# Kernel tuning notes

Measured on AMD Instinct MI355X. Metric: run time of the kernel, lower is better.

## Reference

```python
import jax, jax.numpy as jnp
import numpy as np

N = 250_000        # nodes
E = 8_000_000      # directed edges
F_IN = 16          # dataset.num_features
H = 8              # latent_dim
G = 512            # number of graphs in the batch


def setup_inputs() -> dict:
    key = jax.random.key(0)
    k = jax.random.split(key, 9)
    x = jax.random.normal(k[0], (N, F_IN), dtype=jnp.float32)
    edge_index = jax.random.randint(k[1], (2, E), 0, N, dtype=jnp.int64)
    batch = jnp.sort(jax.random.randint(k[2], (N,), 0, G, dtype=jnp.int64))
    W1 = jax.random.normal(k[3], (F_IN, H), dtype=jnp.float32) * 0.25
    b1 = jax.random.normal(k[4], (H,), dtype=jnp.float32) * 0.1
    W2 = jax.random.normal(k[5], (H, H), dtype=jnp.float32) * 0.35
    b2 = jax.random.normal(k[6], (H,), dtype=jnp.float32) * 0.1
    Wl = jax.random.normal(k[7], (H, 1), dtype=jnp.float32) * 0.35
    bl = jax.random.normal(k[8], (1,), dtype=jnp.float32) * 0.1
    return {"x": x, "edge_index": edge_index, "batch": batch,
            "W1": W1, "b1": b1, "W2": W2, "b2": b2, "Wl": Wl, "bl": bl}


def _gcn_conv(x, src, dst, deg_inv_sqrt, W, b, num_nodes):
    # PyG GCNConv (default): h = x @ W ; msg = norm * h[src] ; scatter-add to dst ; + bias
    h = x @ W                                    # [N, H]
    norm = deg_inv_sqrt[src] * deg_inv_sqrt[dst]  # [E+N]
    msgs = h[src] * norm[:, None]                 # [E+N, H]
    out = jax.ops.segment_sum(msgs, dst, num_segments=num_nodes)
    return out + b


def reference(x, edge_index, batch, W1, b1, W2, b2, Wl, bl):
    num_nodes = x.shape[0]
    loops = jnp.arange(num_nodes, dtype=edge_index.dtype)
    src = jnp.concatenate([edge_index[0], loops])  # self-loops appended
    dst = jnp.concatenate([edge_index[1], loops])
    # symmetric normalization: deg over destination (incl. self-loops)
    deg = jax.ops.segment_sum(jnp.ones_like(dst, dtype=x.dtype), dst,
                              num_segments=num_nodes)
    dis = jnp.where(deg > 0, jax.lax.rsqrt(jnp.maximum(deg, 1.0)), 0.0)
    h = jax.nn.relu(_gcn_conv(x, src, dst, dis, W1, b1, num_nodes))
    h = jax.nn.relu(_gcn_conv(h, src, dst, dis, W2, b2, num_nodes))
    pooled = jax.ops.segment_sum(h, batch, num_segments=G)  # global_add_pool -> [G, H]
    return jax.nn.sigmoid(pooled @ Wl + bl)                 # [G, 1]
```

## Files before the change

### kernel.cpp

```cpp
#include <hip/hip_runtime.h>
#include <math.h>

#define BLK 256
#define CH 4096
#define NBMAX 1024


__global__ void k_init0(int* __restrict__ ghist, float* __restrict__ zacc,
                        int* __restrict__ rowptr, int nb, int ng, int n, int E,
                        int primary) {
  int i = blockIdx.x * BLK + threadIdx.x;
  if (i < nb) ghist[i] = 0;
  if (i < ng) zacc[i] = 0.f;
  if (primary && i == 0) rowptr[n] = E;
}

__global__ void k_hist(const int* __restrict__ dst, int* __restrict__ ghist,
                       int E, int nb, int chunk) {
  __shared__ int h[NBMAX];
  for (int i = threadIdx.x; i < NBMAX; i += BLK) h[i] = 0;
  __syncthreads();
  long long s0 = (long long)blockIdx.x * chunk;
  int c = (int)min((long long)chunk, (long long)E - s0);
  for (int i = threadIdx.x; i < c; i += BLK)
    atomicAdd(&h[dst[s0 + i] >> 8], 1);
  __syncthreads();
  for (int b = threadIdx.x; b < nb; b += BLK)
    if (h[b]) atomicAdd(&ghist[b], h[b]);
}

__global__ void k_scan(const int* __restrict__ ghist, int* __restrict__ base,
                       int* __restrict__ cursor, int nb, int E) {
  __shared__ int temp[BLK];
  int t = threadIdx.x;
  int v[4]; int sm = 0;
  #pragma unroll
  for (int k = 0; k < 4; ++k) {
    int idx = t * 4 + k;
    v[k] = (idx < nb) ? ghist[idx] : 0;
    sm += v[k];
  }
  temp[t] = sm; __syncthreads();
  int inc = sm;
  for (int off = 1; off < BLK; off <<= 1) {
    int u = (t >= off) ? temp[t - off] : 0; __syncthreads();
    inc += u; temp[t] = inc; __syncthreads();
  }
  int run = inc - sm;
  #pragma unroll
  for (int k = 0; k < 4; ++k) {
    int idx = t * 4 + k;
    if (idx < nb) { base[idx] = run; cursor[idx] = run; }
    run += v[k];
  }
  if (t == BLK - 1) base[nb] = E;
}

__global__ void k_bin(const int* __restrict__ src, const int* __restrict__ dst,
                      int* __restrict__ cursor, int* __restrict__ binned,
                      int E, int nb) {
  __shared__ int cnt[NBMAX], cur[NBMAX], gofs[NBMAX], baseA[NBMAX + 1], temp[BLK];
  __shared__ int stage[CH];
  int t = threadIdx.x;
  for (int i = t; i < NBMAX; i += BLK) { cnt[i] = 0; cur[i] = 0; }
  __syncthreads();
  long long s0 = (long long)blockIdx.x * CH;
  int c = (int)min((long long)CH, (long long)E - s0);
  for (int i = t; i < c; i += BLK) atomicAdd(&cnt[dst[s0 + i] >> 8], 1);
  __syncthreads();
  int v[4], sm = 0;
  #pragma unroll
  for (int k = 0; k < 4; ++k) { v[k] = cnt[t * 4 + k]; sm += v[k]; }
  temp[t] = sm; __syncthreads();
  int inc = sm;
  for (int off = 1; off < BLK; off <<= 1) {
    int u = (t >= off) ? temp[t - off] : 0; __syncthreads();
    inc += u; temp[t] = inc; __syncthreads();
  }
  int run = inc - sm;
  #pragma unroll
  for (int k = 0; k < 4; ++k) { baseA[t * 4 + k] = run; run += v[k]; }
  if (t == BLK - 1) baseA[NBMAX] = c;
  __syncthreads();
  for (int b = t; b < nb; b += BLK)
    if (cnt[b]) gofs[b] = atomicAdd(&cursor[b], cnt[b]);
  __syncthreads();
  for (int i = t; i < c; i += BLK) {
    int d = dst[s0 + i];
    int b = d >> 8;
    int r = atomicAdd(&cur[b], 1);
    stage[baseA[b] + r] = (src[s0 + i] << 8) | (d & 255);
  }
  __syncthreads();
  for (int i = t; i < c; i += BLK) {
    int lo = 0, hi = nb;
    while (hi - lo > 1) { int m = (lo + hi) >> 1; if (baseA[m] <= i) lo = m; else hi = m; }
    binned[(size_t)gofs[lo] + (i - baseA[lo])] = stage[i];
  }
}

__global__ void k_sortdis(const int* __restrict__ base, const int* __restrict__ binned,
                          int* __restrict__ csr, int* __restrict__ rowptr,
                          float* __restrict__ dis, int n) {
  __shared__ int cnt[256], loff[256], cur[256], temp[BLK];
  int b = blockIdx.x, t = threadIdx.x;
  cnt[t] = 0; cur[t] = 0;
  __syncthreads();
  int s = base[b], e = base[b + 1];
  for (int i = s + t; i < e; i += BLK) atomicAdd(&cnt[binned[i] & 255], 1);
  __syncthreads();
  int v = cnt[t];
  temp[t] = v; __syncthreads();
  int inc = v;
  for (int off = 1; off < BLK; off <<= 1) {
    int u = (t >= off) ? temp[t - off] : 0; __syncthreads();
    inc += u; temp[t] = inc; __syncthreads();
  }
  loff[t] = inc - v;
  int node = b * 256 + t;
  if (node < n) {
    rowptr[node] = s + inc - v;
    dis[node] = rsqrtf((float)(v + 1));
  }
  __syncthreads();
  for (int i = s + t; i < e; i += BLK) {
    int rec = binned[i];
    int L = rec & 255;
    int p = atomicAdd(&cur[L], 1);
    csr[s + loff[L] + p] = rec >> 8;
  }
}

__global__ void k_gather(const int* __restrict__ rowptr, const int* __restrict__ csr,
                         const float* __restrict__ y, float* __restrict__ acc, int n) {
  int wid = (int)(((long long)blockIdx.x * BLK + threadIdx.x) >> 6);
  if (wid >= n) return;
  int lane = threadIdx.x & 63;
  int e = lane & 31, fq = lane >> 5;
  int start = rowptr[wid], end = rowptr[wid + 1];
  float4 s = make_float4(0.f, 0.f, 0.f, 0.f);
  int k = start + e;
  int sidx = (k < end) ? csr[k] : -1;
  for (int k0 = start; k0 < end; k0 += 32) {
    int nk = k0 + 32 + e;
    int nsidx = (nk < end) ? csr[nk] : -1;
    if (sidx >= 0) {
      const float4 v = *(const float4*)(y + (size_t)sidx * 8 + fq * 4);
      s.x += v.x; s.y += v.y; s.z += v.z; s.w += v.w;
    }
    sidx = nsidx;
  }
  #pragma unroll
  for (int m = 1; m <= 16; m <<= 1) {
    s.x += __shfl_xor(s.x, m);
    s.y += __shfl_xor(s.y, m);
    s.z += __shfl_xor(s.z, m);
    s.w += __shfl_xor(s.w, m);
  }
  if (e == 0) *(float4*)(acc + (size_t)wid * 8 + fq * 4) = s;
}


__global__ void k_degdis(const int* __restrict__ base, const int* __restrict__ binned,
                         float* __restrict__ dis, int n) {
  __shared__ int deg[256];
  int b = blockIdx.x, t = threadIdx.x;
  deg[t] = 1;
  __syncthreads();
  int s = base[b], e = base[b + 1];
  for (int i = s + t; i < e; i += BLK) atomicAdd(&deg[binned[i] & 255], 1);
  __syncthreads();
  int node = b * 256 + t;
  if (node < n) dis[node] = rsqrtf((float)deg[t]);
}

__global__ void k_acc(const int* __restrict__ base, const int* __restrict__ binned,
                      const float* __restrict__ y, float* __restrict__ acc, int n) {
  __shared__ float fa[2048];
  int b = blockIdx.x, t = threadIdx.x;
  for (int i = t; i < 2048; i += BLK) fa[i] = 0.f;
  __syncthreads();
  int s = base[b], e = base[b + 1];
  int j = t & 7;
  for (int i = s + (t >> 3); i < e; i += 32) {
    int rec = binned[i];
    atomicAdd(&fa[(rec & 255) * 8 + j], y[(size_t)(rec >> 8) * 8 + j]);
  }
  __syncthreads();
  int node0 = b * 256;
  int lim = (n - node0 < 256 ? n - node0 : 256) * 8;
  for (int i = t; i < lim; i += BLK) acc[(size_t)node0 * 8 + i] = fa[i];
}


__global__ void k_y1n(const float* __restrict__ x, const float* __restrict__ W1,
                      const float* __restrict__ dis, float* __restrict__ y, int n) {
  __shared__ float sW[128];
  if (threadIdx.x < 128) sW[threadIdx.x] = W1[threadIdx.x];
  __syncthreads();
  int i = blockIdx.x * BLK + threadIdx.x;
  if (i >= n) return;
  const float4* xp = (const float4*)(x + (size_t)i * 16);
  float4 a = xp[0], bb = xp[1], cc = xp[2], d4 = xp[3];
  float xv[16] = {a.x,a.y,a.z,a.w, bb.x,bb.y,bb.z,bb.w,
                  cc.x,cc.y,cc.z,cc.w, d4.x,d4.y,d4.z,d4.w};
  float ds = dis[i];
  float o[8];
  #pragma unroll
  for (int jj = 0; jj < 8; ++jj) {
    float s = 0.f;
    #pragma unroll
    for (int k = 0; k < 16; ++k) s = fmaf(xv[k], sW[k*8 + jj], s);
    o[jj] = ds * s;
  }
  float4* yp = (float4*)(y + (size_t)i * 8);
  yp[0] = make_float4(o[0], o[1], o[2], o[3]);
  yp[1] = make_float4(o[4], o[5], o[6], o[7]);
}

__global__ void k_mid(const float* __restrict__ dis, float* __restrict__ y,
                      float* __restrict__ acc, const float* __restrict__ W2,
                      const float* __restrict__ b1, int n, int zero_acc) {
  __shared__ float sW[64];
  __shared__ float sb[8];
  if (threadIdx.x < 64) sW[threadIdx.x] = W2[threadIdx.x];
  if (threadIdx.x < 8)  sb[threadIdx.x] = b1[threadIdx.x];
  __syncthreads();
  int i = blockIdx.x * BLK + threadIdx.x;
  if (i >= n) return;
  float d = dis[i];
  float4* yp = (float4*)(y + (size_t)i * 8);
  float4* ap = (float4*)(acc + (size_t)i * 8);
  float4 y0 = yp[0], y1v = yp[1], a0 = ap[0], a1 = ap[1];
  float yy[8] = {y0.x,y0.y,y0.z,y0.w, y1v.x,y1v.y,y1v.z,y1v.w};
  float aa[8] = {a0.x,a0.y,a0.z,a0.w, a1.x,a1.y,a1.z,a1.w};
  float hv[8];
  #pragma unroll
  for (int jj = 0; jj < 8; ++jj) hv[jj] = fmaxf(fmaf(d, yy[jj] + aa[jj], sb[jj]), 0.f);
  float o[8];
  #pragma unroll
  for (int jj = 0; jj < 8; ++jj) {
    float s = 0.f;
    #pragma unroll
    for (int k = 0; k < 8; ++k) s = fmaf(hv[k], sW[k*8 + jj], s);
    o[jj] = d * s;
  }
  yp[0] = make_float4(o[0], o[1], o[2], o[3]);
  yp[1] = make_float4(o[4], o[5], o[6], o[7]);
  if (zero_acc) {
    ap[0] = make_float4(0.f, 0.f, 0.f, 0.f);
    ap[1] = make_float4(0.f, 0.f, 0.f, 0.f);
  }
}

__global__ void k_final(const float* __restrict__ dis, const float* __restrict__ y,
                        const float* __restrict__ acc, const float* __restrict__ b2,
                        const float* __restrict__ Wl, const int* __restrict__ batch,
                        float* __restrict__ zacc, int n) {
  __shared__ float sb[8], sw[8];
  if (threadIdx.x < 8) { sb[threadIdx.x] = b2[threadIdx.x]; sw[threadIdx.x] = Wl[threadIdx.x]; }
  __syncthreads();
  int i = blockIdx.x * BLK + threadIdx.x;
  float s = 0.f;
  int g = -1;
  if (i < n) {
    float d = dis[i];
    const float4* yp = (const float4*)(y + (size_t)i * 8);
    const float4* ap = (const float4*)(acc + (size_t)i * 8);
    float4 y0 = yp[0], y1v = yp[1], a0 = ap[0], a1 = ap[1];
    float yy[8] = {y0.x,y0.y,y0.z,y0.w, y1v.x,y1v.y,y1v.z,y1v.w};
    float aa[8] = {a0.x,a0.y,a0.z,a0.w, a1.x,a1.y,a1.z,a1.w};
    #pragma unroll
    for (int jj = 0; jj < 8; ++jj) {
      float h = fmaxf(fmaf(d, yy[jj] + aa[jj], sb[jj]), 0.f);
      s = fmaf(h, sw[jj], s);
    }
    g = batch[i];
  }
  int g0 = __shfl(g, 0);
  bool uni = __all(g == g0);
  if (uni) {
    #pragma unroll
    for (int off = 32; off > 0; off >>= 1) s += __shfl_down(s, off);
    if ((threadIdx.x & 63) == 0 && g0 >= 0) unsafeAtomicAdd(&zacc[g0], s);
  } else if (i < n) {
    unsafeAtomicAdd(&zacc[g], s);
  }
}

__global__ void k_out(const float* __restrict__ zacc, const float* __restrict__ bl,
                      float* __restrict__ out, int ng) {
  int i = blockIdx.x * BLK + threadIdx.x;
  if (i < ng) {
    float z = zacc[i] + bl[0];
    float r;
    if (z >= 0.f) { r = 1.f / (1.f + expf(-z)); }
    else          { float e = expf(z); r = e / (1.f + e); }
    out[i] = r;
  }
}


__global__ void k_init(int* __restrict__ deg, float* __restrict__ acc,
                       float* __restrict__ zacc, int n, int accn, int ng) {
  int jj = blockIdx.x * BLK + threadIdx.x;
  if (jj < accn) acc[jj] = 0.f;
  if (jj < n) deg[jj] = 1;
  if (jj < ng) zacc[jj] = 0.f;
}

__global__ void k_deg(const int* __restrict__ dst, int* __restrict__ deg, int E) {
  int i = blockIdx.x * BLK + threadIdx.x;
  if (i < E) atomicAdd(&deg[dst[i]], 1);
}

__global__ void k_y1(const float* __restrict__ x, const float* __restrict__ W1,
                     int* __restrict__ degdis, float* __restrict__ y, int n) {
  __shared__ float sW[128];
  if (threadIdx.x < 128) sW[threadIdx.x] = W1[threadIdx.x];
  __syncthreads();
  int i = blockIdx.x * BLK + threadIdx.x;
  if (i >= n) return;
  const float4* xp = (const float4*)(x + (size_t)i * 16);
  float4 a = xp[0], bb = xp[1], cc = xp[2], d4 = xp[3];
  float xv[16] = {a.x,a.y,a.z,a.w, bb.x,bb.y,bb.z,bb.w,
                  cc.x,cc.y,cc.z,cc.w, d4.x,d4.y,d4.z,d4.w};
  float ds = rsqrtf((float)degdis[i]);
  float o[8];
  #pragma unroll
  for (int jj = 0; jj < 8; ++jj) {
    float s = 0.f;
    #pragma unroll
    for (int k = 0; k < 16; ++k) s = fmaf(xv[k], sW[k*8 + jj], s);
    o[jj] = ds * s;
  }
  ((float*)degdis)[i] = ds;
  float4* yp = (float4*)(y + (size_t)i * 8);
  yp[0] = make_float4(o[0], o[1], o[2], o[3]);
  yp[1] = make_float4(o[4], o[5], o[6], o[7]);
}

__global__ void k_scatter(const int* __restrict__ src, const int* __restrict__ dst,
                          const float* __restrict__ y, float* __restrict__ acc,
                          long long total) {
  long long t = (long long)blockIdx.x * BLK + threadIdx.x;
  if (t >= total) return;
  int e = (int)(t >> 3);
  int h = (int)(t & 7);
  int s = src[e], d = dst[e];
  unsafeAtomicAdd(&acc[(size_t)d * 8 + h], y[(size_t)s * 8 + h]);
}


static inline size_t alignup(size_t v) { return (v + 255) & ~(size_t)255; }

extern "C" void kernel_launch(void* const* d_in, const int* in_sizes, int n_in,
                              void* d_out, int out_size, void* d_ws, size_t ws_size,
                              hipStream_t stream) {
  const float* x   = (const float*)d_in[0];
  const int*   ei  = (const int*)  d_in[1];
  const int*   bat = (const int*)  d_in[2];
  const float* W1  = (const float*)d_in[3];
  const float* b1  = (const float*)d_in[4];
  const float* W2  = (const float*)d_in[5];
  const float* b2  = (const float*)d_in[6];
  const float* Wl  = (const float*)d_in[7];
  const float* bl  = (const float*)d_in[8];
  float* out = (float*)d_out;

  int n  = in_sizes[0] / 16;
  int E  = in_sizes[1] / 2;
  int ng = out_size;

  const int* src = ei;
  const int* dst = ei + E;

  int nb = (n + 255) >> 8;

  char* wsb = (char*)d_ws;
  size_t offY  = alignup((size_t)n * 4);
  size_t offA  = offY + alignup((size_t)n * 8 * 4);
  size_t offZ  = offA + alignup((size_t)n * 8 * 4);
  size_t offH  = offZ + alignup((size_t)ng * 4);
  size_t offB  = offH + alignup((size_t)NBMAX * 4);
  size_t offCu = offB + alignup((size_t)(NBMAX + 1) * 4);
  size_t offBn = offCu + alignup((size_t)NBMAX * 4);
  size_t offRp = offBn + alignup((size_t)E * 4);
  size_t offCs = offRp + alignup(((size_t)n + 1) * 4);
  size_t need1 = offCs + alignup((size_t)E * 4);
  size_t need2 = offRp;

  float* dis    = (float*)wsb;
  int*   deg    = (int*)wsb;
  float* y      = (float*)(wsb + offY);
  float* acc    = (float*)(wsb + offA);
  float* zacc   = (float*)(wsb + offZ);
  int*   ghist  = (int*)(wsb + offH);
  int*   base   = (int*)(wsb + offB);
  int*   cursor = (int*)(wsb + offCu);
  int*   binned = (int*)(wsb + offBn);
  int*   rowptr = (int*)(wsb + offRp);
  int*   csr    = (int*)(wsb + offCs);

  int gN = (n + BLK - 1) / BLK;
  int gG = (ng + BLK - 1) / BLK;
  int gW = (int)(((long long)n * 64 + BLK - 1) / BLK);

  bool ok_bin = (nb <= NBMAX) && (n < (1 << 23));
  bool tier1 = ok_bin && (ws_size >= need1);
  bool tier2 = ok_bin && (ws_size >= need2);

  if (tier1 || tier2) {
    int histChunk = 4096;
    int gHist = (int)(((long long)E + histChunk - 1) / histChunk);
    int gBin  = (int)(((long long)E + CH - 1) / CH);
    int gI0   = (NBMAX > ng ? NBMAX : ng) / BLK + 1;
    k_init0 <<<gI0, BLK, 0, stream>>>(ghist, zacc, rowptr, NBMAX, ng, n, E, tier1 ? 1 : 0);
    k_hist  <<<gHist, BLK, 0, stream>>>(dst, ghist, E, nb, histChunk);
    k_scan  <<<1, BLK, 0, stream>>>(ghist, base, cursor, nb, E);
    k_bin   <<<gBin, BLK, 0, stream>>>(src, dst, cursor, binned, E, nb);
    if (tier1) {
      k_sortdis<<<nb, BLK, 0, stream>>>(base, binned, csr, rowptr, dis, n);
      k_y1n   <<<gN, BLK, 0, stream>>>(x, W1, dis, y, n);
      k_gather<<<gW, BLK, 0, stream>>>(rowptr, csr, y, acc, n);
      k_mid   <<<gN, BLK, 0, stream>>>(dis, y, acc, W2, b1, n, 0);
      k_gather<<<gW, BLK, 0, stream>>>(rowptr, csr, y, acc, n);
    } else {
      k_degdis<<<nb, BLK, 0, stream>>>(base, binned, dis, n);
      k_y1n   <<<gN, BLK, 0, stream>>>(x, W1, dis, y, n);
      k_acc   <<<nb, BLK, 0, stream>>>(base, binned, y, acc, n);
      k_mid   <<<gN, BLK, 0, stream>>>(dis, y, acc, W2, b1, n, 0);
      k_acc   <<<nb, BLK, 0, stream>>>(base, binned, y, acc, n);
    }
    k_final <<<gN, BLK, 0, stream>>>(dis, y, acc, b2, Wl, bat, zacc, n);
  } else {
    int accn = n * 8;
    long long tot = (long long)E * 8;
    int gInit = (accn + BLK - 1) / BLK;
    int gE    = (E + BLK - 1) / BLK;
    int gS    = (int)((tot + BLK - 1) / BLK);
    k_init   <<<gInit, BLK, 0, stream>>>(deg, acc, zacc, n, accn, ng);
    k_deg    <<<gE, BLK, 0, stream>>>(dst, deg, E);
    k_y1     <<<gN, BLK, 0, stream>>>(x, W1, deg, y, n);
    k_scatter<<<gS, BLK, 0, stream>>>(src, dst, y, acc, tot);
    k_mid    <<<gN, BLK, 0, stream>>>(dis, y, acc, W2, b1, n, 1);
    k_scatter<<<gS, BLK, 0, stream>>>(src, dst, y, acc, tot);
    k_final  <<<gN, BLK, 0, stream>>>(dis, y, acc, b2, Wl, bat, zacc, n);
  }
  k_out<<<gG, BLK, 0, stream>>>(zacc, bl, out, ng);
}
```

Measured before the change: 448.0 us.

## Fuse gather with mid/final epilogues, vectorize binning, replace binary search with bucket table

```diff
diff --git a/kernel.cpp b/kernel.cpp
--- a/kernel.cpp
+++ b/kernel.cpp
@@ -22,8 +22,18 @@
   __syncthreads();
   long long s0 = (long long)blockIdx.x * chunk;
   int c = (int)min((long long)chunk, (long long)E - s0);
-  for (int i = threadIdx.x; i < c; i += BLK)
-    atomicAdd(&h[dst[s0 + i] >> 8], 1);
+  if (c == chunk && (chunk & 3) == 0) {
+    const int4* d4 = (const int4*)(dst + s0);
+    int m = chunk >> 2;
+    for (int i = threadIdx.x; i < m; i += BLK) {
+      int4 v = d4[i];
+      atomicAdd(&h[v.x >> 8], 1); atomicAdd(&h[v.y >> 8], 1);
+      atomicAdd(&h[v.z >> 8], 1); atomicAdd(&h[v.w >> 8], 1);
+    }
+  } else {
+    for (int i = threadIdx.x; i < c; i += BLK)
+      atomicAdd(&h[dst[s0 + i] >> 8], 1);
+  }
   __syncthreads();
   for (int b = threadIdx.x; b < nb; b += BLK)
     if (h[b]) atomicAdd(&ghist[b], h[b]);
@@ -59,43 +69,81 @@
 __global__ void k_bin(const int* __restrict__ src, const int* __restrict__ dst,
                       int* __restrict__ cursor, int* __restrict__ binned,
                       int E, int nb) {
-  __shared__ int cnt[NBMAX], cur[NBMAX], gofs[NBMAX], baseA[NBMAX + 1], temp[BLK];
+  __shared__ int cb[NBMAX + 1];
+  __shared__ int cur[NBMAX];
+  __shared__ int gofs[NBMAX];
+  __shared__ int temp[BLK];
   __shared__ int stage[CH];
+  __shared__ unsigned short bkt[CH];
   int t = threadIdx.x;
-  for (int i = t; i < NBMAX; i += BLK) { cnt[i] = 0; cur[i] = 0; }
+  for (int i = t; i < NBMAX; i += BLK) { cb[i] = 0; cur[i] = 0; }
   __syncthreads();
   long long s0 = (long long)blockIdx.x * CH;
   int c = (int)min((long long)CH, (long long)E - s0);
-  for (int i = t; i < c; i += BLK) atomicAdd(&cnt[dst[s0 + i] >> 8], 1);
-  __syncthreads();
-  int v[4], sm = 0;
-  #pragma unroll
-  for (int k = 0; k < 4; ++k) { v[k] = cnt[t * 4 + k]; sm += v[k]; }
+  if (c == CH) {
+    const int4* d4 = (const int4*)(dst + s0);
+    for (int i = t; i < (CH >> 2); i += BLK) {
+      int4 v = d4[i];
+      atomicAdd(&cb[v.x >> 8], 1); atomicAdd(&cb[v.y >> 8], 1);
+      atomicAdd(&cb[v.z >> 8], 1); atomicAdd(&cb[v.w >> 8], 1);
+    }
+  } else {
+    for (int i = t; i < c; i += BLK) atomicAdd(&cb[dst[s0 + i] >> 8], 1);
+  }
+  __syncthreads();
+  int v[4];
+  #pragma unroll
+  for (int k = 0; k < 4; ++k) v[k] = cb[t * 4 + k];
+  int sm = v[0] + v[1] + v[2] + v[3];
   temp[t] = sm; __syncthreads();
   int inc = sm;
   for (int off = 1; off < BLK; off <<= 1) {
     int u = (t >= off) ? temp[t - off] : 0; __syncthreads();
     inc += u; temp[t] = inc; __syncthreads();
   }
+  #pragma unroll
+  for (int k = 0; k < 4; ++k) {
+    int b = t * 4 + k;
+    if (v[k]) gofs[b] = atomicAdd(&cursor[b], v[k]);
+  }
   int run = inc - sm;
   #pragma unroll
-  for (int k = 0; k < 4; ++k) { baseA[t * 4 + k] = run; run += v[k]; }
-  if (t == BLK - 1) baseA[NBMAX] = c;
-  __syncthreads();
-  for (int b = t; b < nb; b += BLK)
-    if (cnt[b]) gofs[b] = atomicAdd(&cursor[b], cnt[b]);
+  for (int k = 0; k < 4; ++k) { cb[t * 4 + k] = run; run += v[k]; }
+  if (t == BLK - 1) cb[NBMAX] = c;
+  __syncthreads();
+  #pragma unroll
+  for (int k = 0; k < 4; ++k) {
+    int b = t * 4 + k;
+    int s_ = cb[b], e_ = cb[b + 1];
+    if (e_ > s_) {
+      gofs[b] -= s_;
+      for (int i = s_; i < e_; ++i) bkt[i] = (unsigned short)b;
+    }
+  }
+  __syncthreads();
+  if (c == CH) {
+    const int4* d4 = (const int4*)(dst + s0);
+    const int4* s4 = (const int4*)(src + s0);
+    for (int i = t; i < (CH >> 2); i += BLK) {
+      int4 dv = d4[i]; int4 sv = s4[i];
+      int b, r;
+      b = dv.x >> 8; r = atomicAdd(&cur[b], 1); stage[cb[b] + r] = (sv.x << 8) | (dv.x & 255);
+      b = dv.y >> 8; r = atomicAdd(&cur[b], 1); stage[cb[b] + r] = (sv.y << 8) | (dv.y & 255);
+      b = dv.z >> 8; r = atomicAdd(&cur[b], 1); stage[cb[b] + r] = (sv.z << 8) | (dv.z & 255);
+      b = dv.w >> 8; r = atomicAdd(&cur[b], 1); stage[cb[b] + r] = (sv.w << 8) | (dv.w & 255);
+    }
+  } else {
+    for (int i = t; i < c; i += BLK) {
+      int d = dst[s0 + i];
+      int b = d >> 8;
+      int r = atomicAdd(&cur[b], 1);
+      stage[cb[b] + r] = (src[s0 + i] << 8) | (d & 255);
+    }
+  }
   __syncthreads();
   for (int i = t; i < c; i += BLK) {
-    int d = dst[s0 + i];
-    int b = d >> 8;
-    int r = atomicAdd(&cur[b], 1);
-    stage[baseA[b] + r] = (src[s0 + i] << 8) | (d & 255);
-  }
-  __syncthreads();
-  for (int i = t; i < c; i += BLK) {
-    int lo = 0, hi = nb;
-    while (hi - lo > 1) { int m = (lo + hi) >> 1; if (baseA[m] <= i) lo = m; else hi = m; }
-    binned[(size_t)gofs[lo] + (i - baseA[lo])] = stage[i];
+    int b = bkt[i];
+    binned[(size_t)i + gofs[b]] = stage[i];
   }
 }
 
@@ -131,13 +179,19 @@
   }
 }
 
-__global__ void k_gather(const int* __restrict__ rowptr, const int* __restrict__ csr,
-                         const float* __restrict__ y, float* __restrict__ acc, int n) {
-  int wid = (int)(((long long)blockIdx.x * BLK + threadIdx.x) >> 6);
-  if (wid >= n) return;
+__global__ void k_gmid(const int* __restrict__ rowptr, const int* __restrict__ csr,
+                       const float* __restrict__ y, float* __restrict__ y2,
+                       const float* __restrict__ dis, const float* __restrict__ W2,
+                       const float* __restrict__ b1, int n) {
+  __shared__ float sW[64], sb[8];
+  if (threadIdx.x < 64) sW[threadIdx.x] = W2[threadIdx.x];
+  if (threadIdx.x < 8)  sb[threadIdx.x] = b1[threadIdx.x];
+  __syncthreads();
+  int node = (int)(((long long)blockIdx.x * BLK + threadIdx.x) >> 6);
+  if (node >= n) return;
   int lane = threadIdx.x & 63;
   int e = lane & 31, fq = lane >> 5;
-  int start = rowptr[wid], end = rowptr[wid + 1];
+  int start = rowptr[node], end = rowptr[node + 1];
   float4 s = make_float4(0.f, 0.f, 0.f, 0.f);
   int k = start + e;
   int sidx = (k < end) ? csr[k] : -1;
@@ -157,7 +211,73 @@
     s.z += __shfl_xor(s.z, m);
     s.w += __shfl_xor(s.w, m);
   }
-  if (e == 0) *(float4*)(acc + (size_t)wid * 8 + fq * 4) = s;
+  float h0 = __shfl(s.x, lane | 32);
+  float h1 = __shfl(s.y, lane | 32);
+  float h2 = __shfl(s.z, lane | 32);
+  float h3 = __shfl(s.w, lane | 32);
+  int j = lane;
+  float accj = (j == 0) ? s.x : (j == 1) ? s.y : (j == 2) ? s.z : (j == 3) ? s.w
+             : (j == 4) ? h0  : (j == 5) ? h1  : (j == 6) ? h2  : h3;
+  float dsv = dis[node];
+  float yj = (lane < 8) ? y[(size_t)node * 8 + lane] : 0.f;
+  float bj = (lane < 8) ? sb[lane] : 0.f;
+  float hv = fmaxf(fmaf(dsv, accj + yj, bj), 0.f);
+  float o = 0.f;
+  #pragma unroll
+  for (int kk = 0; kk < 8; ++kk) {
+    float hk = __shfl(hv, kk);
+    if (lane < 8) o = fmaf(hk, sW[kk * 8 + lane], o);
+  }
+  if (lane < 8) y2[(size_t)node * 8 + lane] = dsv * o;
+}
+
+__global__ void k_gfin(const int* __restrict__ rowptr, const int* __restrict__ csr,
+                       const float* __restrict__ y2, const float* __restrict__ dis,
+                       const float* __restrict__ b2, const float* __restrict__ Wl,
+                       const int* __restrict__ batch, float* __restrict__ zacc, int n) {
+  __shared__ float sb[8], sw[8];
+  if (threadIdx.x < 8) { sb[threadIdx.x] = b2[threadIdx.x]; sw[threadIdx.x] = Wl[threadIdx.x]; }
+  __syncthreads();
+  int node = (int)(((long long)blockIdx.x * BLK + threadIdx.x) >> 6);
+  if (node >= n) return;
+  int lane = threadIdx.x & 63;
+  int e = lane & 31, fq = lane >> 5;
+  int start = rowptr[node], end = rowptr[node + 1];
+  float4 s = make_float4(0.f, 0.f, 0.f, 0.f);
+  int k = start + e;
+  int sidx = (k < end) ? csr[k] : -1;
+  for (int k0 = start; k0 < end; k0 += 32) {
+    int nk = k0 + 32 + e;
+    int nsidx = (nk < end) ? csr[nk] : -1;
+    if (sidx >= 0) {
+      const float4 v = *(const float4*)(y2 + (size_t)sidx * 8 + fq * 4);
+      s.x += v.x; s.y += v.y; s.z += v.z; s.w += v.w;
+    }
+    sidx = nsidx;
+  }
+  #pragma unroll
+  for (int m = 1; m <= 16; m <<= 1) {
+    s.x += __shfl_xor(s.x, m);
+    s.y += __shfl_xor(s.y, m);
+    s.z += __shfl_xor(s.z, m);
+    s.w += __shfl_xor(s.w, m);
+  }
+  float h0 = __shfl(s.x, lane | 32);
+  float h1 = __shfl(s.y, lane | 32);
+  float h2 = __shfl(s.z, lane | 32);
+  float h3 = __shfl(s.w, lane | 32);
+  int j = lane;
+  float accj = (j == 0) ? s.x : (j == 1) ? s.y : (j == 2) ? s.z : (j == 3) ? s.w
+             : (j == 4) ? h0  : (j == 5) ? h1  : (j == 6) ? h2  : h3;
+  float dsv = dis[node];
+  float yj = (lane < 8) ? y2[(size_t)node * 8 + lane] : 0.f;
+  float bj = (lane < 8) ? sb[lane] : 0.f;
+  float wj = (lane < 8) ? sw[lane] : 0.f;
+  float p = fmaxf(fmaf(dsv, accj + yj, bj), 0.f) * wj;
+  p += __shfl_xor(p, 1);
+  p += __shfl_xor(p, 2);
+  p += __shfl_xor(p, 4);
+  if (lane == 0) unsafeAtomicAdd(&zacc[batch[node]], p);
 }
 
 
@@ -411,7 +531,7 @@
   bool tier2 = ok_bin && (ws_size >= need2);
 
   if (tier1 || tier2) {
-    int histChunk = 4096;
+    int histChunk = 8192;
     int gHist = (int)(((long long)E + histChunk - 1) / histChunk);
     int gBin  = (int)(((long long)E + CH - 1) / CH);
     int gI0   = (NBMAX > ng ? NBMAX : ng) / BLK + 1;
@@ -422,17 +542,16 @@
     if (tier1) {
       k_sortdis<<<nb, BLK, 0, stream>>>(base, binned, csr, rowptr, dis, n);
       k_y1n   <<<gN, BLK, 0, stream>>>(x, W1, dis, y, n);
-      k_gather<<<gW, BLK, 0, stream>>>(rowptr, csr, y, acc, n);
-      k_mid   <<<gN, BLK, 0, stream>>>(dis, y, acc, W2, b1, n, 0);
-      k_gather<<<gW, BLK, 0, stream>>>(rowptr, csr, y, acc, n);
+      k_gmid  <<<gW, BLK, 0, stream>>>(rowptr, csr, y, acc, dis, W2, b1, n);
+      k_gfin  <<<gW, BLK, 0, stream>>>(rowptr, csr, acc, dis, b2, Wl, bat, zacc, n);
     } else {
       k_degdis<<<nb, BLK, 0, stream>>>(base, binned, dis, n);
       k_y1n   <<<gN, BLK, 0, stream>>>(x, W1, dis, y, n);
       k_acc   <<<nb, BLK, 0, stream>>>(base, binned, y, acc, n);
       k_mid   <<<gN, BLK, 0, stream>>>(dis, y, acc, W2, b1, n, 0);
       k_acc   <<<nb, BLK, 0, stream>>>(base, binned, y, acc, n);
-    }
-    k_final <<<gN, BLK, 0, stream>>>(dis, y, acc, b2, Wl, bat, zacc, n);
+      k_final <<<gN, BLK, 0, stream>>>(dis, y, acc, b2, Wl, bat, zacc, n);
+    }
   } else {
     int accn = n * 8;
     long long tot = (long long)E * 8;
```

After: 1.195 ms. 167% more time.
